# Performance work log

Hardware: AMD Instinct MI355X
Metric: run time of the kernel (lower is better)

Reference implementation:

```python
import jax, jax.numpy as jnp
import numpy as np
from jax import lax


def _conv(x, W):
    # NCHW conv, stride 1, SAME padding (padding = kernel//2 in original)
    return lax.conv_general_dilated(x, W, (1, 1), 'SAME',
                                    dimension_numbers=('NCHW', 'OIHW', 'NCHW'))


def _cconv(zr, zi, Wr, Wi, br, bi):
    # complex conv: (zr + i*zi) * (Wr + i*Wi)
    yr = _conv(zr, Wr) - _conv(zi, Wi) + br[None, :, None, None]
    yi = _conv(zr, Wi) + _conv(zi, Wr) + bi[None, :, None, None]
    return yr, yi


def setup_inputs() -> dict:
    key = jax.random.key(0)
    B, C, H, W = 16, 128, 64, 64        # C = 128 total = 64 real + 64 imag channels
    half = C // 2                        # 64 complex channels
    kin = (C + C) // 2                   # (input+hidden)/2 complex input channels = 128
    K = 3
    ks = jax.random.split(key, 20)
    inp = {
        'x':      jax.random.normal(ks[0], (B, C, H, W), jnp.float32),
        'h_prev': jax.random.normal(ks[1], (B, C, H, W), jnp.float32),
        'c_prev': jax.random.normal(ks[2], (B, C, H, W), jnp.float32),
    }
    i = 3
    for g in ('i', 'f', 'o', 'c'):
        inp['Wr_' + g] = jax.random.normal(ks[i], (half, kin, K, K), jnp.float32) * 0.05; i += 1
        inp['Wi_' + g] = jax.random.normal(ks[i], (half, kin, K, K), jnp.float32) * 0.05; i += 1
        inp['br_' + g] = jax.random.normal(ks[i], (half,), jnp.float32) * 0.05; i += 1
        inp['bi_' + g] = jax.random.normal(ks[i], (half,), jnp.float32) * 0.05; i += 1
    return inp


def reference(x, h_prev, c_prev,
              Wr_i, Wi_i, br_i, bi_i,
              Wr_f, Wi_f, br_f, bi_f,
              Wr_o, Wi_o, br_o, bi_o,
              Wr_c, Wi_c, br_c, bi_c):
    C = x.shape[1]
    h = C // 2
    xr, xi = x[:, :h], x[:, h:]
    hr, hi = h_prev[:, :h], h_prev[:, h:]
    cr, ci = c_prev[:, :h], c_prev[:, h:]

    zr = jnp.concatenate([xr, hr], axis=1)   # real part of combined
    zi = jnp.concatenate([xi, hi], axis=1)   # imag part of combined

    # gates: complex conv then split sigmoid / tanh (applied per component)
    i_r, i_i = map(jax.nn.sigmoid, _cconv(zr, zi, Wr_i, Wi_i, br_i, bi_i))
    # f gate conv output is computed but unused in final update (original bug keeps x as f)
    o_r, o_i = map(jax.nn.sigmoid, _cconv(zr, zi, Wr_o, Wi_o, br_o, bi_o))
    ct_r, ct_i = map(jnp.tanh, _cconv(zr, zi, Wr_c, Wi_c, br_c, bi_c))

    # faithful to original: f_r/f_i taken from x, not from conv_f output
    c_new_r = xr * cr - xi * ci + i_r * ct_r - i_i * ct_i
    c_new_i = xr * ci + xi * cr + i_r * ct_i + i_i * ct_r

    t_r = jnp.tanh(c_new_r)
    t_i = jnp.tanh(c_new_i)
    h_new = jnp.concatenate([o_r * t_r - o_i * t_i, o_r * t_i + o_i * t_r], axis=1)
    c_new = jnp.concatenate([c_new_r, c_new_i], axis=1)
    return h_new, c_new
```

## Files before the change

kernel.cpp:

```cpp
#include <hip/hip_runtime.h>
#include <hip/hip_bf16.h>


typedef __attribute__((ext_vector_type(8))) short short8;
typedef __attribute__((ext_vector_type(4))) float floatx4;
typedef __attribute__((ext_vector_type(4))) float float4v;

#define MTOT   65536
#define HSIZE  8388608

__device__ __forceinline__ short f2bf(float f) {
  __hip_bfloat16 h = __float2bfloat16(f);
  return *reinterpret_cast<short*>(&h);
}

__device__ __forceinline__ float bf2f(short s) {
  unsigned u = ((unsigned)(unsigned short)s) << 16;
  return __uint_as_float(u);
}

__device__ __forceinline__ void gload16(const short* g, void* lds) {
  __builtin_amdgcn_global_load_lds(
      (__attribute__((address_space(1))) void*)(g),
      (__attribute__((address_space(3))) void*)(lds), 16, 0, 0);
}

__global__ __launch_bounds__(256) void halo_zero_kernel(short* __restrict__ Zp) {
  int t = blockIdx.x * 256 + threadIdx.x;
  int s   = t & 31;
  int pix = t >> 5;
  int b = pix / 260;
  int r = pix - b * 260;
  int yp, xp;
  if (r < 66)       { yp = 0;               xp = r; }
  else if (r < 132) { yp = 65;              xp = r - 66; }
  else { int r2 = r - 132; yp = 1 + (r2 >> 1); xp = (r2 & 1) * 65; }
  short8 z;
#pragma unroll
  for (int q = 0; q < 8; ++q) z[q] = 0;
  *(short8*)(Zp + (((b * 66 + yp) * 66 + xp) * 256 + s * 8)) = z;
}

__global__ __launch_bounds__(256) void pack_z_kernel(
    const float* __restrict__ xs, const float* __restrict__ hs,
    short* __restrict__ Zp) {
  __shared__ short tile[64 * 72];
  int bid = blockIdx.x;
  int y      = bid & 63;
  int half   = (bid >> 6) & 1;
  int srcSel = (bid >> 7) & 1;
  int b      = bid >> 8;
  const float* src = srcSel ? hs : xs;
  int chBase  = half * 64;
  int cinBase = half * 128 + srcSel * 64;
  int t = threadIdx.x;
  int x4 = t & 15, chq = t >> 4;
#pragma unroll
  for (int p = 0; p < 4; ++p) {
    int ch = p * 16 + chq;
    float4v f = *(const float4v*)(src + (size_t)(b * 128 + chBase + ch) * 4096 + y * 64 + x4 * 4);
#pragma unroll
    for (int e = 0; e < 4; ++e)
      tile[(x4 * 4 + e) * 72 + ch] = f2bf(f[e]);
  }
  __syncthreads();
  int x = t >> 2, seg = t & 3;
  short8 v0 = *(const short8*)(tile + x * 72 + seg * 16);
  short8 v1 = *(const short8*)(tile + x * 72 + seg * 16 + 8);
  size_t outp = ((size_t)(b * 66 + y + 1) * 66 + x + 1) * 256 + cinBase + seg * 16;
  *(short8*)(Zp + outp)     = v0;
  *(short8*)(Zp + outp + 8) = v1;
}

__global__ __launch_bounds__(256) void pack_w_kernel(
    const float* __restrict__ Wr_i, const float* __restrict__ Wi_i,
    const float* __restrict__ Wr_o, const float* __restrict__ Wi_o,
    const float* __restrict__ Wr_c, const float* __restrict__ Wi_c,
    const float* __restrict__ br_i, const float* __restrict__ bi_i,
    const float* __restrict__ br_o, const float* __restrict__ bi_o,
    const float* __restrict__ br_c, const float* __restrict__ bi_c,
    short* __restrict__ Wp, float* __restrict__ bias) {
  int g = blockIdx.x * 256 + threadIdx.x;
  if (g >= 384 * 9 * 256) return;
  int cin = g & 255;
  int tap = (g >> 8) % 9;
  int n   = g / (256 * 9);
  int part = n >> 6, ch = n & 63;
  const float *Wr, *Wi;
  if (part < 2)      { Wr = Wr_i; Wi = Wi_i; }
  else if (part < 4) { Wr = Wr_o; Wi = Wi_o; }
  else               { Wr = Wr_c; Wi = Wi_c; }
  int im = part & 1;
  int ci = cin & 127;
  int second = cin >> 7;
  const float* src = im ? (second ? Wr : Wi) : (second ? Wi : Wr);
  float f = src[(ch * 128 + ci) * 9 + tap];
  if (!im && second) f = -f;
  Wp[(n * 9 + tap) * 256 + cin] = f2bf(f);
  if (g < 384) {
    int p2 = g >> 6, c2 = g & 63;
    const float* bs = (p2 == 0) ? br_i : (p2 == 1) ? bi_i : (p2 == 2) ? br_o
                    : (p2 == 3) ? bi_o : (p2 == 4) ? br_c : bi_c;
    bias[g] = bs[c2];
  }
}

__device__ __forceinline__ void issueA(const short* __restrict__ Wp, int n0,
                                       int ta, int dxa, short8* dst, int tid, int wv) {
  int dy  = ta >> 2;
  int c0  = (ta & 3) * 64;
  int tap = dy * 3 + dxa;
#pragma unroll
  for (int it = 0; it < 4; ++it) {
    int idx = tid + it * 256;
    int row = idx >> 3, p = idx & 7;
    int g = p ^ (row & 7);
    gload16(Wp + ((size_t)((n0 + row) * 9 + tap) * 256 + c0 + g * 8),
            (void*)(dst + (it * 256 + wv * 64)));
  }
}

__device__ __forceinline__ void issueB(const short* __restrict__ Z, int zrow0,
                                       int tb, short8* dst, int tid, int wv) {
  int dy = tb >> 2;
  int c0 = (tb & 3) * 64;
#pragma unroll
  for (int it = 0; it < 4; ++it) {
    int idx = tid + it * 256;
    int r2  = idx >> 9;
    int rem = idx & 511;
    int col = (rem >> 3) + 1;
    int p   = rem & 7;
    int g   = p ^ (col & 7);
    int ygl = zrow0 + dy + r2;
    int idx0 = it * 256 + wv * 64;
    int r2d  = idx0 >> 9;
    int rem0 = idx0 & 511;
    gload16(Z + ((size_t)(ygl * 66 + col) * 256 + c0 + g * 8),
            (void*)(dst + (r2d * 528 + 8 + rem0)));
  }
}

template<int KK, int DXI>
__device__ __forceinline__ void frag_read(const short8* __restrict__ Ab,
                                          const short8* __restrict__ Bb,
                                          short8 (&a)[4], short8 (&bv)[4],
                                          int wch, int r2w, int l15, int l4) {
  int kg = KK * 4 + l4;
#pragma unroll
  for (int i = 0; i < 4; ++i) {
    int row = wch + i * 16 + l15;
    a[i] = Ab[row * 8 + (kg ^ (row & 7))];
  }
#pragma unroll
  for (int j = 0; j < 4; ++j) {
    int col = j * 16 + l15 + DXI;
    bv[j] = Bb[r2w * 528 + col * 8 + (kg ^ (col & 7))];
  }
}

__device__ __forceinline__ void mfma16(const short8 (&a)[4], const short8 (&bv)[4],
                                       floatx4 (&acc)[4][4]) {
#pragma unroll
  for (int i = 0; i < 4; ++i)
#pragma unroll
    for (int j = 0; j < 4; ++j)
      acc[i][j] = __builtin_amdgcn_mfma_f32_16x16x32_bf16(a[i], bv[j], acc[i][j], 0, 0, 0);
}

__global__ __launch_bounds__(256, 2) void conv_gemm(
    const short* __restrict__ Z, const short* __restrict__ Wp,
    const float* __restrict__ bias, __hip_bfloat16* __restrict__ gates) {
  __shared__ short8 As[2][1024];
  __shared__ short8 Bs[2][1056];

  const int tid = threadIdx.x;
  const int wv = tid >> 6, lane = tid & 63;
  const int l15 = lane & 15, l4 = lane >> 4;
  const int m0 = blockIdx.x * 128;
  const int n0 = blockIdx.y * 128;
  const int b  = m0 >> 12;
  const int y0 = (m0 >> 6) & 63;
  const int zrow0 = b * 66 + y0;
  const int wch = (wv & 1) * 64;
  const int r2w = wv >> 1;

  floatx4 acc[4][4];
#pragma unroll
  for (int i = 0; i < 4; ++i)
#pragma unroll
    for (int j = 0; j < 4; ++j)
#pragma unroll
      for (int r = 0; r < 4; ++r) acc[i][j][r] = 0.f;

  short8 af0[4], bf0[4], af1[4], bf1[4];

  if (tid < 64) {
    int buf = tid >> 5, w = tid & 31;
    int r2 = w >> 4, hi = (w >> 3) & 1, p = w & 7;
    short8 z;
#pragma unroll
    for (int q = 0; q < 8; ++q) z[q] = 0;
    Bs[buf][r2 * 528 + (hi ? 520 : 0) + p] = z;
  }
  issueA(Wp, n0, 0, 0, &As[0][0], tid, wv);
  issueB(Z, zrow0, 0, &Bs[0][0], tid, wv);
  issueA(Wp, n0, 0, 1, &As[1][0], tid, wv);
  __builtin_amdgcn_sched_barrier(0);
  asm volatile("s_waitcnt vmcnt(4) lgkmcnt(0)" ::: "memory");
  __builtin_amdgcn_sched_barrier(0);
  __builtin_amdgcn_s_barrier();
  __builtin_amdgcn_sched_barrier(0);
  frag_read<0, 0>(&As[0][0], &Bs[0][0], af0, bf0, wch, r2w, l15, l4);

#define STEP(NW, DOA, TOA, DXA, ABUF, DOB, TOB, BISS, TBUF, TBN, ANXT, DXS, DXN, DON) \
  do {                                                                         \
    frag_read<1, DXS>(&As[ABUF][0], &Bs[TBUF][0], af1, bf1, wch, r2w, l15, l4);\
    __builtin_amdgcn_s_setprio(1);                                             \
    mfma16(af0, bf0, acc);                                                     \
    __builtin_amdgcn_s_setprio(0);                                             \
    __builtin_amdgcn_sched_barrier(0);                                         \
    asm volatile("s_waitcnt vmcnt(" #NW ") lgkmcnt(0)" ::: "memory");          \
    __builtin_amdgcn_sched_barrier(0);                                         \
    __builtin_amdgcn_s_barrier();                                              \
    __builtin_amdgcn_sched_barrier(0);                                         \
    if (DOA) issueA(Wp, n0, t0 + (TOA), (DXA), &As[ABUF][0], tid, wv);         \
    if (DOB) issueB(Z, zrow0, t0 + (TOB), &Bs[BISS][0], tid, wv);              \
    if (DON) frag_read<0, DXN>(&As[ANXT][0], &Bs[TBN][0], af0, bf0,            \
                               wch, r2w, l15, l4);                             \
    __builtin_amdgcn_s_setprio(1);                                             \
    mfma16(af1, bf1, acc);                                                     \
    __builtin_amdgcn_s_setprio(0);                                             \
  } while (0)

  for (int u = 0; u < 5; ++u) {
    int t0 = u * 2;
    STEP(0,  1,  0,  2,  0,   1,  1,  1,   0,   0,  1,   0,  1,  1);
    STEP(4,  1,  1,  0,  1,   0,  0,  0,   0,   0,  0,   1,  2,  1);
    STEP(0,  1,  1,  1,  0,   0,  0,  0,   0,   1,  1,   2,  0,  1);
    STEP(0,  1,  1,  2,  1,   1,  2,  0,   1,   1,  0,   0,  1,  1);
    STEP(4,  1,  2,  0,  0,   0,  0,  0,   1,   1,  1,   1,  2,  1);
    STEP(0,  1,  2,  1,  1,   0,  0,  0,   1,   0,  0,   2,  0,  1);
  }
  {
    int t0 = 10;
    STEP(0,  1,  0,  2,  0,   1,  1,  1,   0,   0,  1,   0,  1,  1);
    STEP(4,  1,  1,  0,  1,   0,  0,  0,   0,   0,  0,   1,  2,  1);
    STEP(0,  1,  1,  1,  0,   0,  0,  0,   0,   1,  1,   2,  0,  1);
    STEP(0,  1,  1,  2,  1,   0,  0,  0,   1,   1,  0,   0,  1,  1);
    STEP(0,  0,  0,  0,  0,   0,  0,  0,   1,   1,  1,   1,  2,  1);
    STEP(0,  0,  0,  0,  1,   0,  0,  0,   1,   0,  0,   2,  0,  0);
  }
#undef STEP

#pragma unroll
  for (int i = 0; i < 4; ++i)
#pragma unroll
    for (int j = 0; j < 4; ++j)
#pragma unroll
      for (int r = 0; r < 4; ++r) {
        int ch = n0 + wch + i * 16 + l4 * 4 + r;
        int px = m0 + r2w * 64 + j * 16 + l15;
        gates[(size_t)ch * MTOT + px] = __float2bfloat16(acc[i][j][r] + bias[ch]);
      }
}

__device__ __forceinline__ float fsig(float v) { return 1.f / (1.f + __expf(-v)); }
__device__ __forceinline__ float ftanh(float v) {
  float e = __expf(2.f * v);
  return 1.f - 2.f / (e + 1.f);
}

__global__ __launch_bounds__(256) void epilogue_kernel(
    const __hip_bfloat16* __restrict__ gates,
    const float* __restrict__ x,
    const float* __restrict__ c_prev,
    float* __restrict__ out) {
  int t = blockIdx.x * 256 + threadIdx.x;
  int ch = t >> 13;
  int m  = (t & 8191) << 3;
  int b = m >> 12, sp = m & 4095;

  size_t gbase = (size_t)ch * MTOT + m;
  short8 gri = *(const short8*)((const short*)gates + gbase);
  short8 gii = *(const short8*)((const short*)gates + gbase + (size_t)64 * MTOT);
  short8 gro = *(const short8*)((const short*)gates + gbase + (size_t)128 * MTOT);
  short8 gio = *(const short8*)((const short*)gates + gbase + (size_t)192 * MTOT);
  short8 grc = *(const short8*)((const short*)gates + gbase + (size_t)256 * MTOT);
  short8 gic = *(const short8*)((const short*)gates + gbase + (size_t)320 * MTOT);

  int base = (b * 128 + ch) * 4096 + sp;
  float xr[8] __attribute__((aligned(16)));
  float xi[8] __attribute__((aligned(16)));
  float cr[8] __attribute__((aligned(16)));
  float ci[8] __attribute__((aligned(16)));
  *(float4v*)(xr)     = *(const float4v*)(x + base);
  *(float4v*)(xr + 4) = *(const float4v*)(x + base + 4);
  *(float4v*)(xi)     = *(const float4v*)(x + base + 64 * 4096);
  *(float4v*)(xi + 4) = *(const float4v*)(x + base + 64 * 4096 + 4);
  *(float4v*)(cr)     = *(const float4v*)(c_prev + base);
  *(float4v*)(cr + 4) = *(const float4v*)(c_prev + base + 4);
  *(float4v*)(ci)     = *(const float4v*)(c_prev + base + 64 * 4096);
  *(float4v*)(ci + 4) = *(const float4v*)(c_prev + base + 64 * 4096 + 4);

  float hr[8] __attribute__((aligned(16)));
  float hi[8] __attribute__((aligned(16)));
  float nr[8] __attribute__((aligned(16)));
  float ni[8] __attribute__((aligned(16)));
#pragma unroll
  for (int q = 0; q < 8; ++q) {
    float i_r = fsig(bf2f(gri[q])), i_i = fsig(bf2f(gii[q]));
    float o_r = fsig(bf2f(gro[q])), o_i = fsig(bf2f(gio[q]));
    float ct_r = ftanh(bf2f(grc[q])), ct_i = ftanh(bf2f(gic[q]));
    float cnr = xr[q] * cr[q] - xi[q] * ci[q] + i_r * ct_r - i_i * ct_i;
    float cni = xr[q] * ci[q] + xi[q] * cr[q] + i_r * ct_i + i_i * ct_r;
    float tr = ftanh(cnr), ti = ftanh(cni);
    hr[q] = o_r * tr - o_i * ti;
    hi[q] = o_r * ti + o_i * tr;
    nr[q] = cnr;
    ni[q] = cni;
  }

  *(float4v*)(out + base)                         = *(const float4v*)(hr);
  *(float4v*)(out + base + 4)                     = *(const float4v*)(hr + 4);
  *(float4v*)(out + base + 64 * 4096)             = *(const float4v*)(hi);
  *(float4v*)(out + base + 64 * 4096 + 4)         = *(const float4v*)(hi + 4);
  *(float4v*)(out + HSIZE + base)                 = *(const float4v*)(nr);
  *(float4v*)(out + HSIZE + base + 4)             = *(const float4v*)(nr + 4);
  *(float4v*)(out + HSIZE + base + 64 * 4096)     = *(const float4v*)(ni);
  *(float4v*)(out + HSIZE + base + 64 * 4096 + 4) = *(const float4v*)(ni + 4);
}

extern "C" void kernel_launch(void* const* d_in, const int* in_sizes, int n_in,
                              void* d_out, int out_size, void* d_ws, size_t ws_size,
                              hipStream_t stream) {
  const float* x = (const float*)d_in[0];
  const float* h = (const float*)d_in[1];

  char* ws = (char*)d_ws;
  short* Zp   = (short*)ws;
  short* Wp   = (short*)(ws + 35684352);
  float* bias = (float*)(ws + 37453824);
  __hip_bfloat16* gates = (__hip_bfloat16*)(ws + 37455360);

  halo_zero_kernel<<<520, 256, 0, stream>>>(Zp);
  pack_z_kernel<<<4096, 256, 0, stream>>>(x, h, Zp);
  pack_w_kernel<<<3456, 256, 0, stream>>>(
      (const float*)d_in[3], (const float*)d_in[4],
      (const float*)d_in[11], (const float*)d_in[12],
      (const float*)d_in[15], (const float*)d_in[16],
      (const float*)d_in[5], (const float*)d_in[6],
      (const float*)d_in[13], (const float*)d_in[14],
      (const float*)d_in[17], (const float*)d_in[18],
      Wp, bias);
  conv_gemm<<<dim3(512, 3), 256, 0, stream>>>(Zp, Wp, bias, gates);
  epilogue_kernel<<<2048, 256, 0, stream>>>(
      gates, (const float*)d_in[0], (const float*)d_in[2],
      (float*)d_out);
}
```

Measured before the change: 317.9 us.

## Load weight fragments directly from global and merge prep kernels into one launch

The three preprocessing kernels (halo zeroing, activation packing, weight packing) are merged into a single launch dispatched by block index. In the conv GEMM, the LDS staging buffer for weights is removed and each lane loads its A fragments directly from global memory (expected to hit cache), while the B tile stays double-buffered in LDS. The hand-tuned STEP schedule with fine-grained vmcnt waits is replaced by a simpler per-tap loop with a full wait and barrier at each iteration. This cuts LDS traffic and kernel launches but puts global-load latency on the MFMA critical path and drops the deeper pipelining.

```diff
diff --git a/kernel.cpp b/kernel.cpp
--- a/kernel.cpp
+++ b/kernel.cpp
@@ -25,54 +25,9 @@
       (__attribute__((address_space(3))) void*)(lds), 16, 0, 0);
 }
 
-__global__ __launch_bounds__(256) void halo_zero_kernel(short* __restrict__ Zp) {
-  int t = blockIdx.x * 256 + threadIdx.x;
-  int s   = t & 31;
-  int pix = t >> 5;
-  int b = pix / 260;
-  int r = pix - b * 260;
-  int yp, xp;
-  if (r < 66)       { yp = 0;               xp = r; }
-  else if (r < 132) { yp = 65;              xp = r - 66; }
-  else { int r2 = r - 132; yp = 1 + (r2 >> 1); xp = (r2 & 1) * 65; }
-  short8 z;
-#pragma unroll
-  for (int q = 0; q < 8; ++q) z[q] = 0;
-  *(short8*)(Zp + (((b * 66 + yp) * 66 + xp) * 256 + s * 8)) = z;
-}
-
-__global__ __launch_bounds__(256) void pack_z_kernel(
+__global__ __launch_bounds__(256) void prep_kernel(
     const float* __restrict__ xs, const float* __restrict__ hs,
-    short* __restrict__ Zp) {
-  __shared__ short tile[64 * 72];
-  int bid = blockIdx.x;
-  int y      = bid & 63;
-  int half   = (bid >> 6) & 1;
-  int srcSel = (bid >> 7) & 1;
-  int b      = bid >> 8;
-  const float* src = srcSel ? hs : xs;
-  int chBase  = half * 64;
-  int cinBase = half * 128 + srcSel * 64;
-  int t = threadIdx.x;
-  int x4 = t & 15, chq = t >> 4;
-#pragma unroll
-  for (int p = 0; p < 4; ++p) {
-    int ch = p * 16 + chq;
-    float4v f = *(const float4v*)(src + (size_t)(b * 128 + chBase + ch) * 4096 + y * 64 + x4 * 4);
-#pragma unroll
-    for (int e = 0; e < 4; ++e)
-      tile[(x4 * 4 + e) * 72 + ch] = f2bf(f[e]);
-  }
-  __syncthreads();
-  int x = t >> 2, seg = t & 3;
-  short8 v0 = *(const short8*)(tile + x * 72 + seg * 16);
-  short8 v1 = *(const short8*)(tile + x * 72 + seg * 16 + 8);
-  size_t outp = ((size_t)(b * 66 + y + 1) * 66 + x + 1) * 256 + cinBase + seg * 16;
-  *(short8*)(Zp + outp)     = v0;
-  *(short8*)(Zp + outp + 8) = v1;
-}
-
-__global__ __launch_bounds__(256) void pack_w_kernel(
+    short* __restrict__ Zp,
     const float* __restrict__ Wr_i, const float* __restrict__ Wi_i,
     const float* __restrict__ Wr_o, const float* __restrict__ Wi_o,
     const float* __restrict__ Wr_c, const float* __restrict__ Wi_c,
@@ -80,43 +35,79 @@
     const float* __restrict__ br_o, const float* __restrict__ bi_o,
     const float* __restrict__ br_c, const float* __restrict__ bi_c,
     short* __restrict__ Wp, float* __restrict__ bias) {
-  int g = blockIdx.x * 256 + threadIdx.x;
-  if (g >= 384 * 9 * 256) return;
-  int cin = g & 255;
-  int tap = (g >> 8) % 9;
-  int n   = g / (256 * 9);
-  int part = n >> 6, ch = n & 63;
-  const float *Wr, *Wi;
-  if (part < 2)      { Wr = Wr_i; Wi = Wi_i; }
-  else if (part < 4) { Wr = Wr_o; Wi = Wi_o; }
-  else               { Wr = Wr_c; Wi = Wi_c; }
-  int im = part & 1;
-  int ci = cin & 127;
-  int second = cin >> 7;
-  const float* src = im ? (second ? Wr : Wi) : (second ? Wi : Wr);
-  float f = src[(ch * 128 + ci) * 9 + tap];
-  if (!im && second) f = -f;
-  Wp[(n * 9 + tap) * 256 + cin] = f2bf(f);
-  if (g < 384) {
-    int p2 = g >> 6, c2 = g & 63;
-    const float* bs = (p2 == 0) ? br_i : (p2 == 1) ? bi_i : (p2 == 2) ? br_o
-                    : (p2 == 3) ? bi_o : (p2 == 4) ? br_c : bi_c;
-    bias[g] = bs[c2];
-  }
-}
-
-__device__ __forceinline__ void issueA(const short* __restrict__ Wp, int n0,
-                                       int ta, int dxa, short8* dst, int tid, int wv) {
-  int dy  = ta >> 2;
-  int c0  = (ta & 3) * 64;
-  int tap = dy * 3 + dxa;
-#pragma unroll
-  for (int it = 0; it < 4; ++it) {
-    int idx = tid + it * 256;
-    int row = idx >> 3, p = idx & 7;
-    int g = p ^ (row & 7);
-    gload16(Wp + ((size_t)((n0 + row) * 9 + tap) * 256 + c0 + g * 8),
-            (void*)(dst + (it * 256 + wv * 64)));
+  __shared__ short tile[64 * 72];
+  int blk = blockIdx.x;
+  int tid = threadIdx.x;
+
+  if (blk < 520) {
+    int t = blk * 256 + tid;
+    int s   = t & 31;
+    int pix = t >> 5;
+    int b = pix / 260;
+    int r = pix - b * 260;
+    int yp, xp;
+    if (r < 66)       { yp = 0;               xp = r; }
+    else if (r < 132) { yp = 65;              xp = r - 66; }
+    else { int r2 = r - 132; yp = 1 + (r2 >> 1); xp = (r2 & 1) * 65; }
+    short8 z;
+#pragma unroll
+    for (int q = 0; q < 8; ++q) z[q] = 0;
+    *(short8*)(Zp + (((b * 66 + yp) * 66 + xp) * 256 + s * 8)) = z;
+    return;
+  }
+
+  if (blk < 520 + 4096) {
+    int bid = blk - 520;
+    int y      = bid & 63;
+    int half   = (bid >> 6) & 1;
+    int srcSel = (bid >> 7) & 1;
+    int b      = bid >> 8;
+    const float* src = srcSel ? hs : xs;
+    int chBase  = half * 64;
+    int cinBase = half * 128 + srcSel * 64;
+    int x4 = tid & 15, chq = tid >> 4;
+#pragma unroll
+    for (int p = 0; p < 4; ++p) {
+      int ch = p * 16 + chq;
+      float4v f = *(const float4v*)(src + (size_t)(b * 128 + chBase + ch) * 4096 + y * 64 + x4 * 4);
+#pragma unroll
+      for (int e = 0; e < 4; ++e)
+        tile[(x4 * 4 + e) * 72 + ch] = f2bf(f[e]);
+    }
+    __syncthreads();
+    int x = tid >> 2, seg = tid & 3;
+    short8 v0 = *(const short8*)(tile + x * 72 + seg * 16);
+    short8 v1 = *(const short8*)(tile + x * 72 + seg * 16 + 8);
+    size_t outp = ((size_t)(b * 66 + y + 1) * 66 + x + 1) * 256 + cinBase + seg * 16;
+    *(short8*)(Zp + outp)     = v0;
+    *(short8*)(Zp + outp + 8) = v1;
+    return;
+  }
+
+  {
+    int g = (blk - 4616) * 256 + tid;
+    if (g >= 384 * 9 * 256) return;
+    int cin = g & 255;
+    int tap = (g >> 8) % 9;
+    int n   = g / (256 * 9);
+    int part = n >> 6, ch = n & 63;
+    const float *Wr, *Wi;
+    if (part < 2)      { Wr = Wr_i; Wi = Wi_i; }
+    else if (part < 4) { Wr = Wr_o; Wi = Wi_o; }
+    else               { Wr = Wr_c; Wi = Wi_c; }
+    int im = part & 1;
+    int ci = cin & 127;
+    int second = cin >> 7;
+    const float* src = im ? (second ? Wr : Wi) : (second ? Wi : Wr);
+    float f = src[(ch * 128 + ci) * 9 + tap];
+    if (!im && second) f = -f;
+    Wp[(n * 9 + tap) * 256 + cin] = f2bf(f);
+    if (g < 384) {
+      int p2 = g >> 6, c2 = g & 63;
+      const float* bs = (p2 == 0) ? br_i : (p2 == 1) ? bi_i : (p2 == 2) ? br_o
+                      : (p2 == 3) ? bi_o : (p2 == 4) ? br_c : bi_c;
+      bias[g] = bs[c2];
+    }
   }
 }
 
@@ -141,17 +132,19 @@
   }
 }
 
+template<int KK>
+__device__ __forceinline__ void loadA(const short* __restrict__ Wp,
+                                      const int (&aoff)[4], int tapc0,
+                                      short8 (&a)[4]) {
+#pragma unroll
+  for (int i = 0; i < 4; ++i)
+    a[i] = *(const short8*)(Wp + aoff[i] + tapc0 + KK * 32);
+}
+
 template<int KK, int DXI>
-__device__ __forceinline__ void frag_read(const short8* __restrict__ Ab,
-                                          const short8* __restrict__ Bb,
-                                          short8 (&a)[4], short8 (&bv)[4],
-                                          int wch, int r2w, int l15, int l4) {
+__device__ __forceinline__ void fragB(const short8* __restrict__ Bb,
+                                      short8 (&bv)[4], int r2w, int l15, int l4) {
   int kg = KK * 4 + l4;
-#pragma unroll
-  for (int i = 0; i < 4; ++i) {
-    int row = wch + i * 16 + l15;
-    a[i] = Ab[row * 8 + (kg ^ (row & 7))];
-  }
 #pragma unroll
   for (int j = 0; j < 4; ++j) {
     int col = j * 16 + l15 + DXI;
@@ -161,17 +154,18 @@
 
 __device__ __forceinline__ void mfma16(const short8 (&a)[4], const short8 (&bv)[4],
                                        floatx4 (&acc)[4][4]) {
+  __builtin_amdgcn_s_setprio(1);
 #pragma unroll
   for (int i = 0; i < 4; ++i)
 #pragma unroll
     for (int j = 0; j < 4; ++j)
       acc[i][j] = __builtin_amdgcn_mfma_f32_16x16x32_bf16(a[i], bv[j], acc[i][j], 0, 0, 0);
+  __builtin_amdgcn_s_setprio(0);
 }
 
 __global__ __launch_bounds__(256, 2) void conv_gemm(
     const short* __restrict__ Z, const short* __restrict__ Wp,
     const float* __restrict__ bias, __hip_bfloat16* __restrict__ gates) {
-  __shared__ short8 As[2][1024];
   __shared__ short8 Bs[2][1056];
 
   const int tid = threadIdx.x;
@@ -185,6 +179,11 @@
   const int wch = (wv & 1) * 64;
   const int r2w = wv >> 1;
 
+  int aoff[4];
+#pragma unroll
+  for (int i = 0; i < 4; ++i)
+    aoff[i] = (n0 + wch + i * 16 + l15) * 2304 + l4 * 8;
+
   floatx4 acc[4][4];
 #pragma unroll
   for (int i = 0; i < 4; ++i)
@@ -203,55 +202,46 @@
     for (int q = 0; q < 8; ++q) z[q] = 0;
     Bs[buf][r2 * 528 + (hi ? 520 : 0) + p] = z;
   }
-  issueA(Wp, n0, 0, 0, &As[0][0], tid, wv);
   issueB(Z, zrow0, 0, &Bs[0][0], tid, wv);
-  issueA(Wp, n0, 0, 1, &As[1][0], tid, wv);
   __builtin_amdgcn_sched_barrier(0);
-  asm volatile("s_waitcnt vmcnt(4) lgkmcnt(0)" ::: "memory");
+  asm volatile("s_waitcnt vmcnt(0) lgkmcnt(0)" ::: "memory");
   __builtin_amdgcn_sched_barrier(0);
   __builtin_amdgcn_s_barrier();
   __builtin_amdgcn_sched_barrier(0);
-  frag_read<0, 0>(&As[0][0], &Bs[0][0], af0, bf0, wch, r2w, l15, l4);
-
-#define STEP(NW, DOA, TOA, DXA, ABUF, DOB, TOB, BISS, TBUF, TBN, ANXT, DXS, DXN, DON) \
-  do {                                                                         \
-    frag_read<1, DXS>(&As[ABUF][0], &Bs[TBUF][0], af1, bf1, wch, r2w, l15, l4);\
-    __builtin_amdgcn_s_setprio(1);                                             \
-    mfma16(af0, bf0, acc);                                                     \
-    __builtin_amdgcn_s_setprio(0);                                             \
-    __builtin_amdgcn_sched_barrier(0);                                         \
-    asm volatile("s_waitcnt vmcnt(" #NW ") lgkmcnt(0)" ::: "memory");          \
-    __builtin_amdgcn_sched_barrier(0);                                         \
-    __builtin_amdgcn_s_barrier();                                              \
-    __builtin_amdgcn_sched_barrier(0);                                         \
-    if (DOA) issueA(Wp, n0, t0 + (TOA), (DXA), &As[ABUF][0], tid, wv);         \
-    if (DOB) issueB(Z, zrow0, t0 + (TOB), &Bs[BISS][0], tid, wv);              \
-    if (DON) frag_read<0, DXN>(&As[ANXT][0], &Bs[TBN][0], af0, bf0,            \
-                               wch, r2w, l15, l4);                             \
-    __builtin_amdgcn_s_setprio(1);                                             \
-    mfma16(af1, bf1, acc);                                                     \
-    __builtin_amdgcn_s_setprio(0);                                             \
-  } while (0)
-
-  for (int u = 0; u < 5; ++u) {
-    int t0 = u * 2;
-    STEP(0,  1,  0,  2,  0,   1,  1,  1,   0,   0,  1,   0,  1,  1);
-    STEP(4,  1,  1,  0,  1,   0,  0,  0,   0,   0,  0,   1,  2,  1);
-    STEP(0,  1,  1,  1,  0,   0,  0,  0,   0,   1,  1,   2,  0,  1);
-    STEP(0,  1,  1,  2,  1,   1,  2,  0,   1,   1,  0,   0,  1,  1);
-    STEP(4,  1,  2,  0,  0,   0,  0,  0,   1,   1,  1,   1,  2,  1);
-    STEP(0,  1,  2,  1,  1,   0,  0,  0,   1,   0,  0,   2,  0,  1);
-  }
-  {
-    int t0 = 10;
-    STEP(0,  1,  0,  2,  0,   1,  1,  1,   0,   0,  1,   0,  1,  1);
-    STEP(4,  1,  1,  0,  1,   0,  0,  0,   0,   0,  0,   1,  2,  1);
-    STEP(0,  1,  1,  1,  0,   0,  0,  0,   0,   1,  1,   2,  0,  1);
-    STEP(0,  1,  1,  2,  1,   0,  0,  0,   1,   1,  0,   0,  1,  1);
-    STEP(0,  0,  0,  0,  0,   0,  0,  0,   1,   1,  1,   1,  2,  1);
-    STEP(0,  0,  0,  0,  1,   0,  0,  0,   1,   0,  0,   2,  0,  0);
-  }
-#undef STEP
+  loadA<0>(Wp, aoff, 0, af0);
+  fragB<0, 0>(&Bs[0][0], bf0, r2w, l15, l4);
+
+  for (int t = 0; t < 12; ++t) {
+    const short8* Bcur = &Bs[t & 1][0];
+    short8*       Bnxt = &Bs[(t & 1) ^ 1][0];
+    const int tc = ((t >> 2) * 3) * 256 + (t & 3) * 64;
+
+    if (t < 11) issueB(Z, zrow0, t + 1, Bnxt, tid, wv);
+
+    loadA<1>(Wp, aoff, tc, af1);        fragB<1, 0>(Bcur, bf1, r2w, l15, l4);
+    mfma16(af0, bf0, acc);
+    loadA<0>(Wp, aoff, tc + 256, af0);  fragB<0, 1>(Bcur, bf0, r2w, l15, l4);
+    mfma16(af1, bf1, acc);
+    loadA<1>(Wp, aoff, tc + 256, af1);  fragB<1, 1>(Bcur, bf1, r2w, l15, l4);
+    mfma16(af0, bf0, acc);
+    loadA<0>(Wp, aoff, tc + 512, af0);  fragB<0, 2>(Bcur, bf0, r2w, l15, l4);
+    mfma16(af1, bf1, acc);
+    loadA<1>(Wp, aoff, tc + 512, af1);  fragB<1, 2>(Bcur, bf1, r2w, l15, l4);
+    mfma16(af0, bf0, acc);
+    mfma16(af1, bf1, acc);
+
+    __builtin_amdgcn_sched_barrier(0);
+    asm volatile("s_waitcnt vmcnt(0)" ::: "memory");
+    __builtin_amdgcn_sched_barrier(0);
+    __builtin_amdgcn_s_barrier();
+    __builtin_amdgcn_sched_barrier(0);
+    if (t < 11) {
+      const int tn = t + 1;
+      const int tcn = ((tn >> 2) * 3) * 256 + (tn & 3) * 64;
+      loadA<0>(Wp, aoff, tcn, af0);
+      fragB<0, 0>(Bnxt, bf0, r2w, l15, l4);
+    }
+  }
 
 #pragma unroll
   for (int i = 0; i < 4; ++i)
@@ -334,18 +324,14 @@
 extern "C" void kernel_launch(void* const* d_in, const int* in_sizes, int n_in,
                               void* d_out, int out_size, void* d_ws, size_t ws_size,
                               hipStream_t stream) {
-  const float* x = (const float*)d_in[0];
-  const float* h = (const float*)d_in[1];
-
   char* ws = (char*)d_ws;
   short* Zp   = (short*)ws;
   short* Wp   = (short*)(ws + 35684352);
   float* bias = (float*)(ws + 37453824);
   __hip_bfloat16* gates = (__hip_bfloat16*)(ws + 37455360);
 
-  halo_zero_kernel<<<520, 256, 0, stream>>>(Zp);
-  pack_z_kernel<<<4096, 256, 0, stream>>>(x, h, Zp);
-  pack_w_kernel<<<3456, 256, 0, stream>>>(
+  prep_kernel<<<8072, 256, 0, stream>>>(
+      (const float*)d_in[0], (const float*)d_in[1], Zp,
       (const float*)d_in[3], (const float*)d_in[4],
       (const float*)d_in[11], (const float*)d_in[12],
       (const float*)d_in[15], (const float*)d_in[16],
```

After: 417.3 us. +31.3%, slower.
